# Performance work log

Measured on AMD Instinct MI355X. Metric: run time of the kernel, lower is better.

## Reference

```python
import jax, jax.numpy as jnp
import numpy as np

NUM_QUBITS = 22
NUM_LAYERS = 4
DIM = 2 ** NUM_QUBITS


def _apply_1q(state, U, q):
    # state: flat [2^n]; apply 2x2 unitary U on wire q (wire 0 = most significant)
    s = state.reshape(2 ** q, 2, -1)
    return jnp.einsum('ab,ibj->iaj', U, s).reshape(-1)


def _apply_cnot_adj(state, q):
    # CNOT with control q, target q+1 (adjacent wires)
    s = state.reshape(2 ** q, 2, 2, -1)
    s = jnp.stack([s[:, 0], s[:, 1, ::-1]], axis=1)
    return s.reshape(-1)


def _rot_mats(theta_x, theta_y, theta_z):
    cx = jnp.cos(theta_x / 2).astype(jnp.complex64)
    sx = jnp.sin(theta_x / 2).astype(jnp.complex64)
    RX = jnp.stack([jnp.stack([cx, -1j * sx]), jnp.stack([-1j * sx, cx])])
    cy = jnp.cos(theta_y / 2).astype(jnp.complex64)
    sy = jnp.sin(theta_y / 2).astype(jnp.complex64)
    RY = jnp.stack([jnp.stack([cy, -sy]), jnp.stack([sy, cy])])
    tz = theta_z.astype(jnp.complex64)
    zero = jnp.zeros((), jnp.complex64)
    RZ = jnp.stack([jnp.stack([jnp.exp(-1j * tz / 2), zero]),
                    jnp.stack([zero, jnp.exp(1j * tz / 2)])])
    return RX, RY, RZ


def _circuit(params, state):
    for l in range(NUM_LAYERS):
        for q in range(NUM_QUBITS):
            RX, RY, RZ = _rot_mats(params[l, q, 0], params[l, q, 1], params[l, q, 2])
            state = _apply_1q(state, RX, q)
            state = _apply_1q(state, RY, q)
            state = _apply_1q(state, RZ, q)
        for q in range(NUM_QUBITS - 1):
            state = _apply_cnot_adj(state, q)
    # <Z_q> for each qubit
    probs = jnp.abs(state) ** 2
    expvals = []
    for q in range(NUM_QUBITS):
        p = probs.reshape(2 ** q, 2, -1)
        expvals.append(p[:, 0].sum() - p[:, 1].sum())
    return jnp.stack(expvals).astype(jnp.float32)


def setup_inputs() -> dict:
    key = jax.random.key(0)
    k1, k2, k3 = jax.random.split(key, 3)
    params = jax.random.normal(k1, (NUM_LAYERS, NUM_QUBITS, 3), dtype=jnp.float32)
    state_re = jax.random.normal(k2, (DIM,), dtype=jnp.float32)
    state_im = jax.random.normal(k3, (DIM,), dtype=jnp.float32)
    return {"params": params, "state_re": state_re, "state_im": state_im}


def reference(params, state_re, state_im):
    state = (state_re + 1j * state_im).astype(jnp.complex64)
    state = state / jnp.sqrt(jnp.sum(jnp.abs(state) ** 2))
    return _circuit(params, state)
```

## Files before the change

### kernel.cpp

```cpp
#include <hip/hip_runtime.h>
#include <math.h>

#define NQ 22
#define DIM (1u << NQ)

typedef float v2f __attribute__((ext_vector_type(2)));


__global__ void k_gates(const float* __restrict__ params, float* __restrict__ U) {
  int t = blockIdx.x * blockDim.x + threadIdx.x;
  if (t >= 88) return;
  const float* p = params + t * 3;
  double hx = 0.5 * (double)p[0], hy = 0.5 * (double)p[1], hz = 0.5 * (double)p[2];
  double cx = cos(hx), sx = sin(hx);
  double cy = cos(hy), sy = sin(hy);
  double cz = cos(hz), sz = sin(hz);
  double m00r = cy * cx, m00i = sy * sx;
  double m01r = -sy * cx, m01i = -cy * sx;
  double m10r = sy * cx, m10i = -cy * sx;
  double m11r = cy * cx, m11i = -sy * sx;
  float* o = U + t * 8;
  o[0] = (float)(cz * m00r + sz * m00i); o[1] = (float)(cz * m00i - sz * m00r);
  o[2] = (float)(cz * m01r + sz * m01i); o[3] = (float)(cz * m01i - sz * m01r);
  o[4] = (float)(cz * m10r - sz * m10i); o[5] = (float)(cz * m10i + sz * m10r);
  o[6] = (float)(cz * m11r - sz * m11i); o[7] = (float)(cz * m11i + sz * m11r);
}

template <int NP>
__device__ __forceinline__ void apply_bit0(v2f RE[NP], v2f IM[NP], const float* __restrict__ u) {
  float u0 = u[0], u1 = u[1], u2 = u[2], u3 = u[3], u4 = u[4], u5 = u[5], u6 = u[6], u7 = u[7];
#pragma unroll
  for (int k = 0; k < NP; ++k) {
    float a0r = RE[k].x, a0i = IM[k].x, a1r = RE[k].y, a1i = IM[k].y;
    float n0r = u0 * a0r - u1 * a0i + u2 * a1r - u3 * a1i;
    float n0i = u0 * a0i + u1 * a0r + u2 * a1i + u3 * a1r;
    float n1r = u4 * a0r - u5 * a0i + u6 * a1r - u7 * a1i;
    float n1i = u4 * a0i + u5 * a0r + u6 * a1i + u7 * a1r;
    RE[k].x = n0r; IM[k].x = n0i; RE[k].y = n1r; IM[k].y = n1i;
  }
}

template <int NP, int PB>
__device__ __forceinline__ void apply_bitP(v2f RE[NP], v2f IM[NP], const float* __restrict__ u) {
  float u0 = u[0], u1 = u[1], u2 = u[2], u3 = u[3], u4 = u[4], u5 = u[5], u6 = u[6], u7 = u[7];
#pragma unroll
  for (int m = 0; m < NP / 2; ++m) {
    int k0 = ((m >> PB) << (PB + 1)) | (m & ((1 << PB) - 1));
    int k1 = k0 | (1 << PB);
    v2f a0r = RE[k0], a0i = IM[k0], a1r = RE[k1], a1i = IM[k1];
    v2f n0r = u0 * a0r - u1 * a0i + u2 * a1r - u3 * a1i;
    v2f n0i = u0 * a0i + u1 * a0r + u2 * a1i + u3 * a1r;
    v2f n1r = u4 * a0r - u5 * a0i + u6 * a1r - u7 * a1i;
    v2f n1i = u4 * a0i + u5 * a0r + u6 * a1i + u7 * a1r;
    RE[k0] = n0r; IM[k0] = n0i; RE[k1] = n1r; IM[k1] = n1i;
  }
}

__device__ __forceinline__ void apply4p(v2f RE[8], v2f IM[8], const float* __restrict__ U,
                                        int l, int wtop) {
  const float* base = U + ((l * 22 + wtop) << 3);
  apply_bit0<8>(RE, IM, base);
  apply_bitP<8, 0>(RE, IM, base - 8);
  apply_bitP<8, 1>(RE, IM, base - 16);
  apply_bitP<8, 2>(RE, IM, base - 24);
}

__device__ __forceinline__ void apply5p(v2f RE[16], v2f IM[16], const float* __restrict__ U,
                                        int l, int wtop) {
  const float* base = U + ((l * 22 + wtop) << 3);
  apply_bit0<16>(RE, IM, base);
  apply_bitP<16, 0>(RE, IM, base - 8);
  apply_bitP<16, 1>(RE, IM, base - 16);
  apply_bitP<16, 2>(RE, IM, base - 24);
  apply_bitP<16, 3>(RE, IM, base - 32);
}

template <typename WI, typename RI>
__device__ __forceinline__ void xchgP(float2* lds2, v2f RE[8], v2f IM[8], WI wi, RI ri) {
  __syncthreads();
#pragma unroll
  for (int d = 0; d < 16; ++d) {
    float2 a;
    if (d & 1) a = make_float2(RE[d >> 1].y, IM[d >> 1].y);
    else       a = make_float2(RE[d >> 1].x, IM[d >> 1].x);
    lds2[wi(d)] = a;
  }
  __syncthreads();
#pragma unroll
  for (int d = 0; d < 16; ++d) {
    float2 a = lds2[ri(d)];
    if (d & 1) { RE[d >> 1].y = a.x; IM[d >> 1].y = a.y; }
    else       { RE[d >> 1].x = a.x; IM[d >> 1].x = a.y; }
  }
}

__global__ __launch_bounds__(256, 4) void k_passA(const float* __restrict__ srcRe,
                                                  const float* __restrict__ srcIm,
                                                  const float2* __restrict__ src2,
                                                  float2* __restrict__ dst,
                                                  const float* __restrict__ U,
                                                  int layer, int first) {
  __shared__ float2 lds2[4096];
  const int t = threadIdx.x;
  const unsigned H = blockIdx.x;
  v2f RE[8], IM[8];
  if (first) {
    const unsigned jbase = (H << 12) | ((unsigned)t << 4);
    const float4* r4 = (const float4*)(srcRe + jbase);
    const float4* i4 = (const float4*)(srcIm + jbase);
#pragma unroll
    for (int k = 0; k < 4; ++k) {
      float4 r = r4[k], m = i4[k];
      RE[2 * k].x     = r.x; RE[2 * k].y     = r.y;
      IM[2 * k].x     = m.x; IM[2 * k].y     = m.y;
      RE[2 * k + 1].x = r.z; RE[2 * k + 1].y = r.w;
      IM[2 * k + 1].x = m.z; IM[2 * k + 1].y = m.w;
    }
  } else {
    const unsigned b = (H << 8) | (unsigned)t;
    const unsigned w = b ^ (b >> 1);
    const float4* s4 = (const float4*)(src2 + ((size_t)w << 4));
    float4 raw[8];
#pragma unroll
    for (int k = 0; k < 8; ++k) raw[k] = s4[k];
    v2f WR[8], WIm[8];
#pragma unroll
    for (int k = 0; k < 8; ++k) {
      WR[k].x = raw[k].x; WR[k].y = raw[k].z;
      WIm[k].x = raw[k].y; WIm[k].y = raw[k].w;
    }
    if (b & 1) {
#pragma unroll
      for (int k = 0; k < 4; ++k) {
        v2f tr = WR[k]; WR[k] = WR[k + 4]; WR[k + 4] = tr;
        v2f ti = WIm[k]; WIm[k] = WIm[k + 4]; WIm[k + 4] = ti;
      }
    }
#pragma unroll
    for (int k = 0; k < 8; ++k) {
      const int s = (2 * k) ^ k;
      const int j = s >> 1;
      if (s & 1) {
        RE[k].x = WR[j].y; RE[k].y = WR[j].x;
        IM[k].x = WIm[j].y; IM[k].y = WIm[j].x;
      } else {
        RE[k] = WR[j]; IM[k] = WIm[j];
      }
    }
  }
  auto wA = [&](int d) { unsigned j = ((unsigned)t << 4) | (unsigned)d; return (int)(j ^ (j >> 4)); };
  auto rB = [&](int d) { unsigned j = (((unsigned)t >> 4) << 8) | ((unsigned)d << 4) | ((unsigned)t & 15); return (int)(j ^ (j >> 4)); };
  auto rC = [&](int d) { unsigned j = ((unsigned)d << 8) | (unsigned)t; return (int)(j ^ (j >> 4)); };

  apply4p(RE, IM, U, layer, 21);
  xchgP(lds2, RE, IM, wA, rB);
  apply4p(RE, IM, U, layer, 17);
  xchgP(lds2, RE, IM, rB, rC);
  apply4p(RE, IM, U, layer, 13);
  float2* dp = dst + (((size_t)H << 3) | (unsigned)(t & 7));
#pragma unroll
  for (int d = 0; d < 16; ++d) {
    float2 a;
    if (d & 1) a = make_float2(RE[d >> 1].y, IM[d >> 1].y);
    else       a = make_float2(RE[d >> 1].x, IM[d >> 1].x);
    dp[(((size_t)d << 5) | (unsigned)(t >> 3)) << 13] = a;
  }
}

__device__ __forceinline__ int pb_idx(unsigned h, unsigned c) {
  return (int)(((h << 3) | c) ^ (((h >> 5) & 3u) << 3));
}

__global__ __launch_bounds__(256, 4) void k_passB(const float2* __restrict__ src,
                                                  float2* __restrict__ dst,
                                                  const float* __restrict__ U,
                                                  int layer) {
  __shared__ float lds[8192];
  const int t = threadIdx.x;
  const unsigned c = (unsigned)(t & 7), u = (unsigned)(t >> 3);
  const unsigned mid = blockIdx.x;
  const float2* sp = src + (((size_t)mid << 13) | c);
  v2f RE[16], IM[16];
#pragma unroll
  for (int d = 0; d < 32; ++d) {
    unsigned h = u | ((unsigned)d << 5);
    float2 a = sp[(size_t)h << 3];
    if (d & 1) { RE[d >> 1].y = a.x; IM[d >> 1].y = a.y; }
    else       { RE[d >> 1].x = a.x; IM[d >> 1].x = a.y; }
  }
  apply5p(RE, IM, U, layer, 4);
  __syncthreads();
#pragma unroll
  for (int d = 0; d < 32; ++d) {
    unsigned h = u | ((unsigned)d << 5);
    lds[pb_idx(h, c)] = (d & 1) ? RE[d >> 1].y : RE[d >> 1].x;
  }
  __syncthreads();
#pragma unroll
  for (int d = 0; d < 32; ++d) {
    unsigned h = (unsigned)d | (u << 5);
    float a = lds[pb_idx(h, c)];
    if (d & 1) RE[d >> 1].y = a; else RE[d >> 1].x = a;
  }
  __syncthreads();
#pragma unroll
  for (int d = 0; d < 32; ++d) {
    unsigned h = u | ((unsigned)d << 5);
    lds[pb_idx(h, c)] = (d & 1) ? IM[d >> 1].y : IM[d >> 1].x;
  }
  __syncthreads();
#pragma unroll
  for (int d = 0; d < 32; ++d) {
    unsigned h = (unsigned)d | (u << 5);
    float a = lds[pb_idx(h, c)];
    if (d & 1) IM[d >> 1].y = a; else IM[d >> 1].x = a;
  }
  apply5p(RE, IM, U, layer, 9);
#pragma unroll
  for (int d = 0; d < 32; ++d) {
    unsigned h = (unsigned)d | (u << 5);
    float2 a;
    if (d & 1) a = make_float2(RE[d >> 1].y, IM[d >> 1].y);
    else       a = make_float2(RE[d >> 1].x, IM[d >> 1].x);
    dst[((size_t)h << 12) | (mid << 3) | c] = a;
  }
}

__global__ __launch_bounds__(256, 4) void k_passB_ev(const float2* __restrict__ src,
                                                     const float* __restrict__ U,
                                                     float* __restrict__ partials,
                                                     int layer) {
  __shared__ float lds[8192];
  const int t = threadIdx.x;
  const unsigned c = (unsigned)(t & 7), u = (unsigned)(t >> 3);
  const unsigned mid = blockIdx.x;
  const float2* sp = src + (((size_t)mid << 13) | c);
  v2f RE[16], IM[16];
#pragma unroll
  for (int d = 0; d < 32; ++d) {
    unsigned h = u | ((unsigned)d << 5);
    float2 a = sp[(size_t)h << 3];
    if (d & 1) { RE[d >> 1].y = a.x; IM[d >> 1].y = a.y; }
    else       { RE[d >> 1].x = a.x; IM[d >> 1].x = a.y; }
  }
  apply5p(RE, IM, U, layer, 4);
  __syncthreads();
#pragma unroll
  for (int d = 0; d < 32; ++d) {
    unsigned h = u | ((unsigned)d << 5);
    lds[pb_idx(h, c)] = (d & 1) ? RE[d >> 1].y : RE[d >> 1].x;
  }
  __syncthreads();
#pragma unroll
  for (int d = 0; d < 32; ++d) {
    unsigned h = (unsigned)d | (u << 5);
    float a = lds[pb_idx(h, c)];
    if (d & 1) RE[d >> 1].y = a; else RE[d >> 1].x = a;
  }
  __syncthreads();
#pragma unroll
  for (int d = 0; d < 32; ++d) {
    unsigned h = u | ((unsigned)d << 5);
    lds[pb_idx(h, c)] = (d & 1) ? IM[d >> 1].y : IM[d >> 1].x;
  }
  __syncthreads();
#pragma unroll
  for (int d = 0; d < 32; ++d) {
    unsigned h = (unsigned)d | (u << 5);
    float a = lds[pb_idx(h, c)];
    if (d & 1) IM[d >> 1].y = a; else IM[d >> 1].x = a;
  }
  apply5p(RE, IM, U, layer, 9);

  v2f PS[16];
#pragma unroll
  for (int k = 0; k < 16; ++k) PS[k] = RE[k] * RE[k] + IM[k] * IM[k];
  v2f S4[8], B4[8];
#pragma unroll
  for (int k = 0; k < 8; ++k) { S4[k] = PS[k] + PS[k + 8]; B4[k] = PS[k] - PS[k + 8]; }
  float Tot = 0.f, W4 = 0.f;
#pragma unroll
  for (int k = 0; k < 8; ++k) { Tot += S4[k].x + S4[k].y; W4 += B4[k].x + B4[k].y; }
  v2f B3[4];
#pragma unroll
  for (int k = 0; k < 4; ++k) B3[k] = B4[k] - B4[k + 4];
  float W3 = (B3[0].x + B3[0].y) + (B3[1].x + B3[1].y) + (B3[2].x + B3[2].y) + (B3[3].x + B3[3].y);
  v2f B2[2];
  B2[0] = B3[0] - B3[2]; B2[1] = B3[1] - B3[3];
  float W2 = (B2[0].x + B2[0].y) + (B2[1].x + B2[1].y);
  v2f B1 = B2[0] - B2[1];
  float W1 = B1.x + B1.y;
  float W0 = B1.x - B1.y;

  unsigned lowfull = (mid << 3) | c;
  unsigned y = lowfull; y ^= y >> 1; y ^= y >> 2; y ^= y >> 4; y ^= y >> 8;
  unsigned pu = (unsigned)__popc(u) & 1u;
  float acc[22];
#pragma unroll
  for (int q = 0; q <= 4; ++q)
    acc[q] = ((unsigned)__popc(u >> (4 - q)) & 1u) ? -Tot : Tot;
  {
    float W[5] = {W0, W1, W2, W3, W4};
#pragma unroll
    for (int q = 5; q <= 9; ++q)
      acc[q] = pu ? -W[9 - q] : W[9 - q];
  }
#pragma unroll
  for (int q = 10; q <= 21; ++q)
    acc[q] = (((y >> (21 - q)) ^ pu) & 1u) ? -W0 : W0;

  __syncthreads();
  float* red = lds;
  const int lane = t & 63, wv = t >> 6;
#pragma unroll
  for (int q = 0; q < 22; ++q) {
    float s = acc[q];
    for (int off = 32; off > 0; off >>= 1) s += __shfl_down(s, off, 64);
    if (lane == 0) red[wv * 23 + q] = s;
  }
  {
    float s = Tot;
    for (int off = 32; off > 0; off >>= 1) s += __shfl_down(s, off, 64);
    if (lane == 0) red[wv * 23 + 22] = s;
  }
  __syncthreads();
  if (t < 23) {
    float s = 0.f;
#pragma unroll
    for (int w = 0; w < 4; ++w) s += red[w * 23 + t];
    partials[t * 512 + mid] = s;
  }
}

__global__ void k_final(const float* __restrict__ partials, float* __restrict__ out) {
  __shared__ double res[32];
  const int t = threadIdx.x;
  const int r = t >> 3, l8 = t & 7;
  if (r < 23) {
    double s = 0.0;
    const float* p = partials + r * 512 + l8 * 64;
    for (int k = 0; k < 64; ++k) s += (double)p[k];
    for (int off = 4; off > 0; off >>= 1) s += __shfl_down(s, off, 8);
    if (l8 == 0) res[r] = s;
  }
  __syncthreads();
  if (t < 22) out[t] = (float)(res[t] / res[22]);
}

extern "C" void kernel_launch(void* const* d_in, const int* in_sizes, int n_in,
                              void* d_out, int out_size, void* d_ws, size_t ws_size,
                              hipStream_t stream) {
  const float* params = (const float*)d_in[0];
  const float* sre = (const float*)d_in[1];
  const float* sim = (const float*)d_in[2];
  float* out = (float*)d_out;
  char* ws = (char*)d_ws;
  float* U = (float*)ws;
  float* partials = (float*)(ws + 4096);
  float2* buf0 = (float2*)(ws + 131072);
  float2* buf1 = buf0 + DIM;

  k_gates<<<1, 128, 0, stream>>>(params, U);
  k_passA<<<1024, 256, 0, stream>>>(sre, sim, nullptr, buf0, U, 0, 1);
  k_passB<<<512, 256, 0, stream>>>(buf0, buf1, U, 0);
  for (int l = 1; l < 3; ++l) {
    k_passA<<<1024, 256, 0, stream>>>(nullptr, nullptr, buf1, buf0, U, l, 0);
    k_passB<<<512, 256, 0, stream>>>(buf0, buf1, U, l);
  }
  k_passA<<<1024, 256, 0, stream>>>(nullptr, nullptr, buf1, buf0, U, 3, 0);
  k_passB_ev<<<512, 256, 0, stream>>>(buf0, U, partials, 3);
  k_final<<<1, 256, 0, stream>>>(partials, out);
}
```

Measured before the change: 219.7 us.

## Move CNOT gray permutation into passB stores, merge LDS transposes, fuse final reduction

PassB now writes its output at Gray-code permuted addresses, so the CNOT-chain permutation is applied at store time and passA loads contiguous float4s with no shuffling. The two separate real/imag LDS transposes are merged into one float2 transpose with a new swizzle, using 64KB LDS and launch bounds lowered to 2 blocks per CU. Blocks are remapped across XCDs by interleaving block ids. The final reduction kernel is folded into passB_ev with an atomic last-block counter. The scattered permuted stores and lower occupancy may cost memory efficiency.

```diff
diff --git a/kernel.cpp b/kernel.cpp
--- a/kernel.cpp
+++ b/kernel.cpp
@@ -7,8 +7,15 @@
 typedef float v2f __attribute__((ext_vector_type(2)));
 
 
-__global__ void k_gates(const float* __restrict__ params, float* __restrict__ U) {
+__device__ __forceinline__ unsigned igray(unsigned x) {
+  x ^= x >> 1; x ^= x >> 2; x ^= x >> 4; x ^= x >> 8; x ^= x >> 16;
+  return x;
+}
+
+__global__ void k_gates(const float* __restrict__ params, float* __restrict__ U,
+                        unsigned* __restrict__ cnt) {
   int t = blockIdx.x * blockDim.x + threadIdx.x;
+  if (t == 0) *cnt = 0;
   if (t >= 88) return;
   const float* p = params + t * 3;
   double hx = 0.5 * (double)p[0], hy = 0.5 * (double)p[1], hz = 0.5 * (double)p[2];
@@ -102,7 +109,8 @@
                                                   int layer, int first) {
   __shared__ float2 lds2[4096];
   const int t = threadIdx.x;
-  const unsigned H = blockIdx.x;
+  const unsigned bid = blockIdx.x;
+  const unsigned H = (bid & 7u) * (gridDim.x >> 3) + (bid >> 3);
   v2f RE[8], IM[8];
   if (first) {
     const unsigned jbase = (H << 12) | ((unsigned)t << 4);
@@ -117,35 +125,12 @@
       IM[2 * k + 1].x = m.z; IM[2 * k + 1].y = m.w;
     }
   } else {
-    const unsigned b = (H << 8) | (unsigned)t;
-    const unsigned w = b ^ (b >> 1);
-    const float4* s4 = (const float4*)(src2 + ((size_t)w << 4));
-    float4 raw[8];
-#pragma unroll
-    for (int k = 0; k < 8; ++k) raw[k] = s4[k];
-    v2f WR[8], WIm[8];
+    const float4* s4 = (const float4*)(src2 + (((size_t)H << 12) | ((size_t)t << 4)));
 #pragma unroll
     for (int k = 0; k < 8; ++k) {
-      WR[k].x = raw[k].x; WR[k].y = raw[k].z;
-      WIm[k].x = raw[k].y; WIm[k].y = raw[k].w;
-    }
-    if (b & 1) {
-#pragma unroll
-      for (int k = 0; k < 4; ++k) {
-        v2f tr = WR[k]; WR[k] = WR[k + 4]; WR[k + 4] = tr;
-        v2f ti = WIm[k]; WIm[k] = WIm[k + 4]; WIm[k + 4] = ti;
-      }
-    }
-#pragma unroll
-    for (int k = 0; k < 8; ++k) {
-      const int s = (2 * k) ^ k;
-      const int j = s >> 1;
-      if (s & 1) {
-        RE[k].x = WR[j].y; RE[k].y = WR[j].x;
-        IM[k].x = WIm[j].y; IM[k].y = WIm[j].x;
-      } else {
-        RE[k] = WR[j]; IM[k] = WIm[j];
-      }
+      float4 a = s4[k];
+      RE[k].x = a.x; IM[k].x = a.y;
+      RE[k].y = a.z; IM[k].y = a.w;
     }
   }
   auto wA = [&](int d) { unsigned j = ((unsigned)t << 4) | (unsigned)d; return (int)(j ^ (j >> 4)); };
@@ -167,18 +152,19 @@
   }
 }
 
-__device__ __forceinline__ int pb_idx(unsigned h, unsigned c) {
-  return (int)(((h << 3) | c) ^ (((h >> 5) & 3u) << 3));
-}
-
-__global__ __launch_bounds__(256, 4) void k_passB(const float2* __restrict__ src,
+__device__ __forceinline__ int pbf(unsigned e) {
+  return (int)(e ^ (((e >> 8) & 7u) << 3));
+}
+
+__global__ __launch_bounds__(256, 2) void k_passB(const float2* __restrict__ src,
                                                   float2* __restrict__ dst,
                                                   const float* __restrict__ U,
                                                   int layer) {
-  __shared__ float lds[8192];
+  __shared__ float2 lds2[8192];
   const int t = threadIdx.x;
   const unsigned c = (unsigned)(t & 7), u = (unsigned)(t >> 3);
-  const unsigned mid = blockIdx.x;
+  const unsigned bid = blockIdx.x;
+  const unsigned mid = (bid & 7u) * (gridDim.x >> 3) + (bid >> 3);
   const float2* sp = src + (((size_t)mid << 13) | c);
   v2f RE[16], IM[16];
 #pragma unroll
@@ -189,51 +175,45 @@
     else       { RE[d >> 1].x = a.x; IM[d >> 1].x = a.y; }
   }
   apply5p(RE, IM, U, layer, 4);
-  __syncthreads();
-#pragma unroll
-  for (int d = 0; d < 32; ++d) {
-    unsigned h = u | ((unsigned)d << 5);
-    lds[pb_idx(h, c)] = (d & 1) ? RE[d >> 1].y : RE[d >> 1].x;
-  }
-  __syncthreads();
-#pragma unroll
-  for (int d = 0; d < 32; ++d) {
-    unsigned h = (unsigned)d | (u << 5);
-    float a = lds[pb_idx(h, c)];
-    if (d & 1) RE[d >> 1].y = a; else RE[d >> 1].x = a;
-  }
-  __syncthreads();
-#pragma unroll
-  for (int d = 0; d < 32; ++d) {
-    unsigned h = u | ((unsigned)d << 5);
-    lds[pb_idx(h, c)] = (d & 1) ? IM[d >> 1].y : IM[d >> 1].x;
-  }
-  __syncthreads();
-#pragma unroll
-  for (int d = 0; d < 32; ++d) {
-    unsigned h = (unsigned)d | (u << 5);
-    float a = lds[pb_idx(h, c)];
-    if (d & 1) IM[d >> 1].y = a; else IM[d >> 1].x = a;
+#pragma unroll
+  for (int d = 0; d < 32; ++d) {
+    unsigned e = ((u | ((unsigned)d << 5)) << 3) | c;
+    float2 a;
+    if (d & 1) a = make_float2(RE[d >> 1].y, IM[d >> 1].y);
+    else       a = make_float2(RE[d >> 1].x, IM[d >> 1].x);
+    lds2[pbf(e)] = a;
+  }
+  __syncthreads();
+#pragma unroll
+  for (int d = 0; d < 32; ++d) {
+    unsigned e = (((unsigned)d | (u << 5)) << 3) | c;
+    float2 a = lds2[pbf(e)];
+    if (d & 1) { RE[d >> 1].y = a.x; IM[d >> 1].y = a.y; }
+    else       { RE[d >> 1].x = a.x; IM[d >> 1].x = a.y; }
   }
   apply5p(RE, IM, U, layer, 9);
-#pragma unroll
-  for (int d = 0; d < 32; ++d) {
-    unsigned h = (unsigned)d | (u << 5);
-    float2 a;
-    if (d & 1) a = make_float2(RE[d >> 1].y, IM[d >> 1].y);
-    else       a = make_float2(RE[d >> 1].x, IM[d >> 1].x);
-    dst[((size_t)h << 12) | (mid << 3) | c] = a;
-  }
-}
-
-__global__ __launch_bounds__(256, 4) void k_passB_ev(const float2* __restrict__ src,
+  const unsigned Tb = igray((u << 17) | (mid << 3) | c);
+#pragma unroll
+  for (int d = 0; d < 32; ++d) {
+    float2 a;
+    if (d & 1) a = make_float2(RE[d >> 1].y, IM[d >> 1].y);
+    else       a = make_float2(RE[d >> 1].x, IM[d >> 1].x);
+    dst[Tb ^ igray((unsigned)d << 12)] = a;
+  }
+}
+
+__global__ __launch_bounds__(256, 2) void k_passB_ev(const float2* __restrict__ src,
                                                      const float* __restrict__ U,
                                                      float* __restrict__ partials,
+                                                     float* __restrict__ outp,
+                                                     unsigned* __restrict__ cnt,
                                                      int layer) {
-  __shared__ float lds[8192];
+  __shared__ float2 lds2[8192];
+  __shared__ unsigned lastf;
   const int t = threadIdx.x;
   const unsigned c = (unsigned)(t & 7), u = (unsigned)(t >> 3);
-  const unsigned mid = blockIdx.x;
+  const unsigned bid = blockIdx.x;
+  const unsigned mid = (bid & 7u) * (gridDim.x >> 3) + (bid >> 3);
   const float2* sp = src + (((size_t)mid << 13) | c);
   v2f RE[16], IM[16];
 #pragma unroll
@@ -244,31 +224,21 @@
     else       { RE[d >> 1].x = a.x; IM[d >> 1].x = a.y; }
   }
   apply5p(RE, IM, U, layer, 4);
-  __syncthreads();
-#pragma unroll
-  for (int d = 0; d < 32; ++d) {
-    unsigned h = u | ((unsigned)d << 5);
-    lds[pb_idx(h, c)] = (d & 1) ? RE[d >> 1].y : RE[d >> 1].x;
-  }
-  __syncthreads();
-#pragma unroll
-  for (int d = 0; d < 32; ++d) {
-    unsigned h = (unsigned)d | (u << 5);
-    float a = lds[pb_idx(h, c)];
-    if (d & 1) RE[d >> 1].y = a; else RE[d >> 1].x = a;
-  }
-  __syncthreads();
-#pragma unroll
-  for (int d = 0; d < 32; ++d) {
-    unsigned h = u | ((unsigned)d << 5);
-    lds[pb_idx(h, c)] = (d & 1) ? IM[d >> 1].y : IM[d >> 1].x;
-  }
-  __syncthreads();
-#pragma unroll
-  for (int d = 0; d < 32; ++d) {
-    unsigned h = (unsigned)d | (u << 5);
-    float a = lds[pb_idx(h, c)];
-    if (d & 1) IM[d >> 1].y = a; else IM[d >> 1].x = a;
+#pragma unroll
+  for (int d = 0; d < 32; ++d) {
+    unsigned e = ((u | ((unsigned)d << 5)) << 3) | c;
+    float2 a;
+    if (d & 1) a = make_float2(RE[d >> 1].y, IM[d >> 1].y);
+    else       a = make_float2(RE[d >> 1].x, IM[d >> 1].x);
+    lds2[pbf(e)] = a;
+  }
+  __syncthreads();
+#pragma unroll
+  for (int d = 0; d < 32; ++d) {
+    unsigned e = (((unsigned)d | (u << 5)) << 3) | c;
+    float2 a = lds2[pbf(e)];
+    if (d & 1) { RE[d >> 1].y = a.x; IM[d >> 1].y = a.y; }
+    else       { RE[d >> 1].x = a.x; IM[d >> 1].x = a.y; }
   }
   apply5p(RE, IM, U, layer, 9);
 
@@ -310,7 +280,7 @@
     acc[q] = (((y >> (21 - q)) ^ pu) & 1u) ? -W0 : W0;
 
   __syncthreads();
-  float* red = lds;
+  float* red = (float*)lds2;
   const int lane = t & 63, wv = t >> 6;
 #pragma unroll
   for (int q = 0; q < 22; ++q) {
@@ -330,21 +300,25 @@
     for (int w = 0; w < 4; ++w) s += red[w * 23 + t];
     partials[t * 512 + mid] = s;
   }
-}
-
-__global__ void k_final(const float* __restrict__ partials, float* __restrict__ out) {
-  __shared__ double res[32];
-  const int t = threadIdx.x;
-  const int r = t >> 3, l8 = t & 7;
-  if (r < 23) {
-    double s = 0.0;
-    const float* p = partials + r * 512 + l8 * 64;
-    for (int k = 0; k < 64; ++k) s += (double)p[k];
-    for (int off = 4; off > 0; off >>= 1) s += __shfl_down(s, off, 8);
-    if (l8 == 0) res[r] = s;
-  }
-  __syncthreads();
-  if (t < 22) out[t] = (float)(res[t] / res[22]);
+
+  __threadfence();
+  __syncthreads();
+  if (t == 0) lastf = (atomicAdd(cnt, 1u) == 511u) ? 1u : 0u;
+  __syncthreads();
+  if (lastf) {
+    __threadfence();
+    double* res = (double*)lds2;
+    const int r = t >> 3, l8 = t & 7;
+    if (r < 23) {
+      double s = 0.0;
+      const float* p = partials + r * 512 + l8 * 64;
+      for (int k = 0; k < 64; ++k) s += (double)p[k];
+      for (int off = 4; off > 0; off >>= 1) s += __shfl_down(s, off, 8);
+      if (l8 == 0) res[r] = s;
+    }
+    __syncthreads();
+    if (t < 22) outp[t] = (float)(res[t] / res[22]);
+  }
 }
 
 extern "C" void kernel_launch(void* const* d_in, const int* in_sizes, int n_in,
@@ -357,10 +331,11 @@
   char* ws = (char*)d_ws;
   float* U = (float*)ws;
   float* partials = (float*)(ws + 4096);
+  unsigned* cnt = (unsigned*)(ws + 65536);
   float2* buf0 = (float2*)(ws + 131072);
   float2* buf1 = buf0 + DIM;
 
-  k_gates<<<1, 128, 0, stream>>>(params, U);
+  k_gates<<<1, 128, 0, stream>>>(params, U, cnt);
   k_passA<<<1024, 256, 0, stream>>>(sre, sim, nullptr, buf0, U, 0, 1);
   k_passB<<<512, 256, 0, stream>>>(buf0, buf1, U, 0);
   for (int l = 1; l < 3; ++l) {
@@ -368,6 +343,5 @@
     k_passB<<<512, 256, 0, stream>>>(buf0, buf1, U, l);
   }
   k_passA<<<1024, 256, 0, stream>>>(nullptr, nullptr, buf1, buf0, U, 3, 0);
-  k_passB_ev<<<512, 256, 0, stream>>>(buf0, U, partials, 3);
-  k_final<<<1, 256, 0, stream>>>(partials, out);
-}
+  k_passB_ev<<<512, 256, 0, stream>>>(buf0, U, partials, out, cnt, 3);
+}
```

Result: slower. 246.6 us (+12.2%).
